# Performance work log

Hardware: AMD Instinct MI355X
Metric: run time of the kernel (lower is better)

Reference implementation:

```python
import jax, jax.numpy as jnp
import numpy as np

EPS = 1e-6


def _csmd(X, M):
    # cross squared Mahalanobis distances: [N, N]
    prod = ((X @ M) * X).sum(axis=1)
    cross = X @ M @ X.T
    return prod[:, None] + prod[None, :] - 2.0 * cross


def setup_inputs() -> dict:
    key = jax.random.key(0)
    kx, kg, ky = jax.random.split(key, 3)
    N, D = 384, 128
    X = jax.random.normal(kx, (N, D), dtype=jnp.float32)
    G = jax.random.normal(kg, (D, D), dtype=jnp.float32)
    y = jax.random.randint(ky, (N,), 0, 10, dtype=jnp.int64)
    return {"X": X, "G": G, "y": y}


def reference(X, G, y):
    N = X.shape[0]
    M = G.T @ G
    csmd = _csmd(X, M)                                  # [N, N]
    # diff[i, j, k] = relu(csmd[i, k] - csmd[i, j])
    diff = jnp.maximum(csmd[:, None, :] - csmd[:, :, None], 0.0)  # [N, N, N]
    csmd2 = _csmd(X, M.T @ M)                           # [N, N]
    denom = jnp.maximum(2.0 * jnp.sqrt(jnp.maximum(csmd2, EPS)), EPS)  # [N, N] over (j, k)
    margins = diff / denom[None, :, :]                  # [N, N, N]
    same = y[None, :] == y[:, None]                     # [N, N], symmetric
    zero_ij = (~same) | jnp.eye(N, dtype=bool)          # zero where y[i]!=y[j] or i==j
    margins = jnp.where(zero_ij[:, :, None], 0.0, margins)
    inner_max = margins.max(axis=1)                     # [N, N] over (i, k)
    inner_max = jnp.where(same, jnp.inf, inner_max)     # exclude same-class k
    return inner_max.min(axis=1)                        # [N]
```

## Files before the change

kernel.cpp:

```cpp
#include <hip/hip_runtime.h>
#include <math.h>

#define NN 384
#define DD 128
#define NTILE (NN / 16)
#define EPSF 1e-6f

__global__ void __launch_bounds__(128) k_A(const float* __restrict__ X,
                                           const float* __restrict__ G,
                                           float* __restrict__ A,
                                           float* __restrict__ prod,
                                           float* __restrict__ p2) {
    __shared__ float Xi[DD];
    __shared__ float Bs[DD];
    __shared__ float rp[2], rq[2];
    const int i = blockIdx.x;
    const int t = threadIdx.x;

    if (t < DD / 4) ((float4*)Xi)[t] = ((const float4*)(X + (size_t)i * DD))[t];
    __syncthreads();

    float b = 0.f;
    const float* gr = G + (size_t)t * DD;
#pragma unroll
    for (int d = 0; d < DD; d += 4) {
        float4 g = *(const float4*)(gr + d);
        b = fmaf(g.x, Xi[d + 0], b);
        b = fmaf(g.y, Xi[d + 1], b);
        b = fmaf(g.z, Xi[d + 2], b);
        b = fmaf(g.w, Xi[d + 3], b);
    }
    Bs[t] = b;
    __syncthreads();

    float a = 0.f;
#pragma unroll 8
    for (int c = 0; c < DD; ++c)
        a = fmaf(Bs[c], G[(size_t)c * DD + t], a);
    A[(size_t)i * DD + t] = a;

    float pp = b * b, qq = a * a;
#pragma unroll
    for (int off = 32; off > 0; off >>= 1) {
        pp += __shfl_down(pp, off);
        qq += __shfl_down(qq, off);
    }
    if ((t & 63) == 0) { rp[t >> 6] = pp; rq[t >> 6] = qq; }
    __syncthreads();
    if (t == 0) { prod[i] = rp[0] + rp[1]; p2[i] = rq[0] + rq[1]; }
}

__global__ void __launch_bounds__(256) k_csmd(const float* __restrict__ X,
                                              const float* __restrict__ A,
                                              const float* __restrict__ prod,
                                              const float* __restrict__ p2,
                                              float* __restrict__ csmd,
                                              float* __restrict__ invd) {
    const int ti = blockIdx.y, tk = blockIdx.x;
    if (ti > tk) return;
    __shared__ float Ai[16][20], Xk[16][20], Ak[16][20];
    __shared__ float Tc[16][17], Tv[16][17];
    const int tx = threadIdx.x, ty = threadIdx.y;
    const int k0 = tk * 16, i0 = ti * 16;
    float dA = 0.f, dAA = 0.f;
    for (int d0 = 0; d0 < DD; d0 += 16) {
        Ai[ty][tx] = A[(size_t)(i0 + ty) * DD + d0 + tx];
        Xk[ty][tx] = X[(size_t)(k0 + ty) * DD + d0 + tx];
        Ak[ty][tx] = A[(size_t)(k0 + ty) * DD + d0 + tx];
        __syncthreads();
#pragma unroll
        for (int t4 = 0; t4 < 16; t4 += 4) {
            float4 aa = *(const float4*)&Ai[ty][t4];
            float4 xx = *(const float4*)&Xk[tx][t4];
            float4 ak = *(const float4*)&Ak[tx][t4];
            dA  = fmaf(aa.x, xx.x, dA);  dA  = fmaf(aa.y, xx.y, dA);
            dA  = fmaf(aa.z, xx.z, dA);  dA  = fmaf(aa.w, xx.w, dA);
            dAA = fmaf(aa.x, ak.x, dAA); dAA = fmaf(aa.y, ak.y, dAA);
            dAA = fmaf(aa.z, ak.z, dAA); dAA = fmaf(aa.w, ak.w, dAA);
        }
        __syncthreads();
    }
    const int i = i0 + ty, k = k0 + tx;
    const float c1 = prod[i] + prod[k] - 2.f * dA;
    const float c2 = p2[i] + p2[k] - 2.f * dAA;
    const float inv = 1.f / fmaxf(2.f * sqrtf(fmaxf(c2, EPSF)), EPSF);
    csmd[(size_t)i * NN + k] = c1;
    invd[(size_t)i * NN + k] = inv;
    if (ti != tk) {
        Tc[tx][ty] = c1;
        Tv[tx][ty] = inv;
        __syncthreads();
        csmd[(size_t)(k0 + ty) * NN + i0 + tx] = Tc[ty][tx];
        invd[(size_t)(k0 + ty) * NN + i0 + tx] = Tv[ty][tx];
    }
}

__global__ void __launch_bounds__(NN) k_cube(const float* __restrict__ csmd,
                                             const float* __restrict__ invd,
                                             const int* __restrict__ y,
                                             float* __restrict__ out) {
    __shared__ float cvals[NN];
    __shared__ int   jidx[NN];
    __shared__ float red[NN];
    __shared__ int   cnt;
    const int i = blockIdx.x;
    const int t = threadIdx.x;
    const int yi = y[i];
    if (t == 0) cnt = 0;
    __syncthreads();
    const float cit = csmd[(size_t)i * NN + t];
    const int yt = y[t];
    if (yt == yi && t != i) {
        int p = atomicAdd(&cnt, 1);
        cvals[p] = cit;
        jidx[p]  = t;
    }
    __syncthreads();
    const int c = cnt;
    float m = 0.f;
    const float* invcol = invd + t;
    for (int jj = 0; jj < c; ++jj) {
        float dlt = fmaxf(cit - cvals[jj], 0.f);
        m = fmaxf(m, dlt * invcol[(size_t)jidx[jj] * NN]);
    }
    if (yt == yi) m = __builtin_inff();
    red[t] = m;
    __syncthreads();
    if (t < 128) red[t] = fminf(red[t], fminf(red[t + 128], red[t + 256]));
    __syncthreads();
    if (t < 64) {
        float v = fminf(red[t], red[t + 64]);
#pragma unroll
        for (int off = 32; off > 0; off >>= 1)
            v = fminf(v, __shfl_down(v, off));
        if (t == 0) out[i] = v;
    }
}

extern "C" void kernel_launch(void* const* d_in, const int* in_sizes, int n_in,
                              void* d_out, int out_size, void* d_ws, size_t ws_size,
                              hipStream_t stream) {
    const float* X = (const float*)d_in[0];
    const float* G = (const float*)d_in[1];
    const int*   y = (const int*)d_in[2];

    float* ws   = (float*)d_ws;
    float* A    = ws;
    float* prod = A + NN * DD;
    float* p2   = prod + NN;
    float* csmd = p2 + NN;
    float* invd = csmd + NN * NN;
    float* out  = (float*)d_out;

    k_A   <<<dim3(NN), dim3(DD), 0, stream>>>(X, G, A, prod, p2);
    k_csmd<<<dim3(NTILE, NTILE), dim3(16, 16), 0, stream>>>(X, A, prod, p2, csmd, invd);
    k_cube<<<dim3(NN), dim3(NN), 0, stream>>>(csmd, invd, y, out);
}
```

Before: 30.07 us.

## Fuse distance and margin stages into a per-class, per-k-chunk kernel

Replaces the full N×N csmd/invd materialization and the cube kernel with one kernel launched over (k-chunk, class). Each block gathers the rows of one class and recomputes the needed same-class distances and inverse denominators in shared memory, using B = G·x so that x M xᵀ = B·Bᵀ. Per-row minima are combined with a float-as-int atomicMin into an output that k_A first sets to infinity. This drops one launch and the global round trip of two N×N buffers, at the price of redundant GEMM work per block. It also hardcodes 10 classes and a cap of 64 rows per class, beyond which rows are silently truncated.

After: 38.86 us. +29.2%, slower.

```diff
diff --git a/kernel.cpp b/kernel.cpp
--- a/kernel.cpp
+++ b/kernel.cpp
@@ -3,14 +3,20 @@
 
 #define NN 384
 #define DD 128
-#define NTILE (NN / 16)
+#define KCH 16
+#define NCHUNK (NN / KCH)
+#define NCLS 10
+#define CMAX 64
+#define STR 132
 #define EPSF 1e-6f
 
 __global__ void __launch_bounds__(128) k_A(const float* __restrict__ X,
                                            const float* __restrict__ G,
+                                           float* __restrict__ B,
                                            float* __restrict__ A,
                                            float* __restrict__ prod,
-                                           float* __restrict__ p2) {
+                                           float* __restrict__ p2,
+                                           float* __restrict__ out) {
     __shared__ float Xi[DD];
     __shared__ float Bs[DD];
     __shared__ float rp[2], rq[2];
@@ -31,6 +37,7 @@
         b = fmaf(g.w, Xi[d + 3], b);
     }
     Bs[t] = b;
+    B[(size_t)i * DD + t] = b;
     __syncthreads();
 
     float a = 0.f;
@@ -47,93 +54,177 @@
     }
     if ((t & 63) == 0) { rp[t >> 6] = pp; rq[t >> 6] = qq; }
     __syncthreads();
-    if (t == 0) { prod[i] = rp[0] + rp[1]; p2[i] = rq[0] + rq[1]; }
+    if (t == 0) {
+        prod[i] = rp[0] + rp[1];
+        p2[i]   = rq[0] + rq[1];
+        out[i]  = __builtin_inff();
+    }
 }
 
-__global__ void __launch_bounds__(256) k_csmd(const float* __restrict__ X,
-                                              const float* __restrict__ A,
-                                              const float* __restrict__ prod,
-                                              const float* __restrict__ p2,
-                                              float* __restrict__ csmd,
-                                              float* __restrict__ invd) {
-    const int ti = blockIdx.y, tk = blockIdx.x;
-    if (ti > tk) return;
-    __shared__ float Ai[16][20], Xk[16][20], Ak[16][20];
-    __shared__ float Tc[16][17], Tv[16][17];
-    const int tx = threadIdx.x, ty = threadIdx.y;
-    const int k0 = tk * 16, i0 = ti * 16;
-    float dA = 0.f, dAA = 0.f;
-    for (int d0 = 0; d0 < DD; d0 += 16) {
-        Ai[ty][tx] = A[(size_t)(i0 + ty) * DD + d0 + tx];
-        Xk[ty][tx] = X[(size_t)(k0 + ty) * DD + d0 + tx];
-        Ak[ty][tx] = A[(size_t)(k0 + ty) * DD + d0 + tx];
-        __syncthreads();
-#pragma unroll
-        for (int t4 = 0; t4 < 16; t4 += 4) {
-            float4 aa = *(const float4*)&Ai[ty][t4];
-            float4 xx = *(const float4*)&Xk[tx][t4];
-            float4 ak = *(const float4*)&Ak[tx][t4];
-            dA  = fmaf(aa.x, xx.x, dA);  dA  = fmaf(aa.y, xx.y, dA);
-            dA  = fmaf(aa.z, xx.z, dA);  dA  = fmaf(aa.w, xx.w, dA);
-            dAA = fmaf(aa.x, ak.x, dAA); dAA = fmaf(aa.y, ak.y, dAA);
-            dAA = fmaf(aa.z, ak.z, dAA); dAA = fmaf(aa.w, ak.w, dAA);
-        }
-        __syncthreads();
-    }
-    const int i = i0 + ty, k = k0 + tx;
-    const float c1 = prod[i] + prod[k] - 2.f * dA;
-    const float c2 = p2[i] + p2[k] - 2.f * dAA;
-    const float inv = 1.f / fmaxf(2.f * sqrtf(fmaxf(c2, EPSF)), EPSF);
-    csmd[(size_t)i * NN + k] = c1;
-    invd[(size_t)i * NN + k] = inv;
-    if (ti != tk) {
-        Tc[tx][ty] = c1;
-        Tv[tx][ty] = inv;
-        __syncthreads();
-        csmd[(size_t)(k0 + ty) * NN + i0 + tx] = Tc[ty][tx];
-        invd[(size_t)(k0 + ty) * NN + i0 + tx] = Tv[ty][tx];
-    }
-}
-
-__global__ void __launch_bounds__(NN) k_cube(const float* __restrict__ csmd,
-                                             const float* __restrict__ invd,
-                                             const int* __restrict__ y,
-                                             float* __restrict__ out) {
-    __shared__ float cvals[NN];
-    __shared__ int   jidx[NN];
-    __shared__ float red[NN];
+__global__ void __launch_bounds__(256) k_margin(const float* __restrict__ B,
+                                                const float* __restrict__ A,
+                                                const float* __restrict__ prod,
+                                                const float* __restrict__ p2,
+                                                const int* __restrict__ y,
+                                                float* __restrict__ out) {
+    __shared__ float SC[CMAX][STR];
+    __shared__ float SK[KCH][STR];
+    __shared__ float ccc[CMAX][CMAX];
+    __shared__ float cck[CMAX][KCH];
+    __shared__ float ick[CMAX][KCH];
+    __shared__ float pc[CMAX], qc[CMAX];
+    __shared__ float pk[KCH], qk[KCH];
+    __shared__ int   yk[KCH];
+    __shared__ int   list[CMAX];
     __shared__ int   cnt;
-    const int i = blockIdx.x;
-    const int t = threadIdx.x;
-    const int yi = y[i];
+
+    const int t  = threadIdx.x;
+    const int tx = t & 15, ty = t >> 4;
+    const int C  = blockIdx.y;
+    const int k0 = blockIdx.x * KCH;
+
     if (t == 0) cnt = 0;
     __syncthreads();
-    const float cit = csmd[(size_t)i * NN + t];
-    const int yt = y[t];
-    if (yt == yi && t != i) {
-        int p = atomicAdd(&cnt, 1);
-        cvals[p] = cit;
-        jidx[p]  = t;
-    }
-    __syncthreads();
-    const int c = cnt;
-    float m = 0.f;
-    const float* invcol = invd + t;
-    for (int jj = 0; jj < c; ++jj) {
-        float dlt = fmaxf(cit - cvals[jj], 0.f);
-        m = fmaxf(m, dlt * invcol[(size_t)jidx[jj] * NN]);
-    }
-    if (yt == yi) m = __builtin_inff();
-    red[t] = m;
-    __syncthreads();
-    if (t < 128) red[t] = fminf(red[t], fminf(red[t + 128], red[t + 256]));
-    __syncthreads();
-    if (t < 64) {
-        float v = fminf(red[t], red[t + 64]);
-#pragma unroll
-        for (int off = 32; off > 0; off >>= 1)
-            v = fminf(v, __shfl_down(v, off));
-        if (t == 0) out[i] = v;
+    for (int r = t; r < NN; r += 256) {
+        if (y[r] == C) {
+            int p = atomicAdd(&cnt, 1);
+            if (p < CMAX) {
+                list[p] = r;
+                pc[p] = prod[r];
+                qc[p] = p2[r];
+            }
+        }
+    }
+    if (t < KCH) {
+        pk[t] = prod[k0 + t];
+        qk[t] = p2[k0 + t];
+        yk[t] = y[k0 + t];
+    }
+    __syncthreads();
+    const int nc = min(cnt, CMAX);
+
+    for (int idx = t; idx < nc * 32; idx += 256) {
+        int r = idx >> 5, q = idx & 31;
+        *(float4*)&SC[r][q * 4] = ((const float4*)(B + (size_t)list[r] * DD))[q];
+    }
+    for (int idx = t; idx < KCH * 32; idx += 256) {
+        int r = idx >> 5, q = idx & 31;
+        *(float4*)&SK[r][q * 4] = ((const float4*)(B + (size_t)(k0 + r) * DD))[q];
+    }
+    __syncthreads();
+
+    {
+        const int i0 = ty * 4;
+        if (i0 < nc) {
+            float acc[4][4] = {};
+#pragma unroll 2
+            for (int d = 0; d < DD; d += 4) {
+                float4 bi[4], bj[4];
+#pragma unroll
+                for (int a = 0; a < 4; ++a) bi[a] = *(const float4*)&SC[i0 + a][d];
+#pragma unroll
+                for (int rj = 0; rj < 4; ++rj) bj[rj] = *(const float4*)&SC[tx + 16 * rj][d];
+#pragma unroll
+                for (int a = 0; a < 4; ++a)
+#pragma unroll
+                    for (int rj = 0; rj < 4; ++rj) {
+                        acc[a][rj] = fmaf(bi[a].x, bj[rj].x, acc[a][rj]);
+                        acc[a][rj] = fmaf(bi[a].y, bj[rj].y, acc[a][rj]);
+                        acc[a][rj] = fmaf(bi[a].z, bj[rj].z, acc[a][rj]);
+                        acc[a][rj] = fmaf(bi[a].w, bj[rj].w, acc[a][rj]);
+                    }
+            }
+#pragma unroll
+            for (int a = 0; a < 4; ++a) {
+                const int i = i0 + a;
+                if (i < nc)
+#pragma unroll
+                    for (int rj = 0; rj < 4; ++rj) {
+                        const int j = tx + 16 * rj;
+                        ccc[i][j] = pc[i] + pc[j] - 2.f * acc[a][rj];
+                    }
+            }
+        }
+    }
+    {
+        float acc[4] = {};
+#pragma unroll 2
+        for (int d = 0; d < DD; d += 4) {
+            float4 bk = *(const float4*)&SK[tx][d];
+#pragma unroll
+            for (int r = 0; r < 4; ++r) {
+                float4 bi = *(const float4*)&SC[ty + 16 * r][d];
+                acc[r] = fmaf(bi.x, bk.x, acc[r]);
+                acc[r] = fmaf(bi.y, bk.y, acc[r]);
+                acc[r] = fmaf(bi.z, bk.z, acc[r]);
+                acc[r] = fmaf(bi.w, bk.w, acc[r]);
+            }
+        }
+#pragma unroll
+        for (int r = 0; r < 4; ++r) {
+            const int i = ty + 16 * r;
+            if (i < nc) cck[i][tx] = pc[i] + pk[tx] - 2.f * acc[r];
+        }
+    }
+    __syncthreads();
+
+    for (int idx = t; idx < nc * 32; idx += 256) {
+        int r = idx >> 5, q = idx & 31;
+        *(float4*)&SC[r][q * 4] = ((const float4*)(A + (size_t)list[r] * DD))[q];
+    }
+    for (int idx = t; idx < KCH * 32; idx += 256) {
+        int r = idx >> 5, q = idx & 31;
+        *(float4*)&SK[r][q * 4] = ((const float4*)(A + (size_t)(k0 + r) * DD))[q];
+    }
+    if (t < nc) ccc[t][t] = __builtin_inff();
+    __syncthreads();
+
+    {
+        float acc[4] = {};
+#pragma unroll 2
+        for (int d = 0; d < DD; d += 4) {
+            float4 ak = *(const float4*)&SK[tx][d];
+#pragma unroll
+            for (int r = 0; r < 4; ++r) {
+                float4 ai = *(const float4*)&SC[ty + 16 * r][d];
+                acc[r] = fmaf(ai.x, ak.x, acc[r]);
+                acc[r] = fmaf(ai.y, ak.y, acc[r]);
+                acc[r] = fmaf(ai.z, ak.z, acc[r]);
+                acc[r] = fmaf(ai.w, ak.w, acc[r]);
+            }
+        }
+#pragma unroll
+        for (int r = 0; r < 4; ++r) {
+            const int j = ty + 16 * r;
+            if (j < nc) {
+                float c2 = qc[j] + qk[tx] - 2.f * acc[r];
+                ick[j][tx] = 1.f / fmaxf(2.f * sqrtf(fmaxf(c2, EPSF)), EPSF);
+            }
+        }
+    }
+    __syncthreads();
+
+    {
+        const bool kex = (yk[tx] == C);
+#pragma unroll
+        for (int r = 0; r < 4; ++r) {
+            const int i = ty + 16 * r;
+            float m = 0.f;
+            if (i < nc) {
+                const float cik = cck[i][tx];
+#pragma unroll 4
+                for (int j = 0; j < nc; ++j) {
+                    float dlt = fmaxf(cik - ccc[i][j], 0.f);
+                    m = fmaxf(m, dlt * ick[j][tx]);
+                }
+            }
+            if (kex) m = __builtin_inff();
+#pragma unroll
+            for (int off = 1; off < 16; off <<= 1)
+                m = fminf(m, __shfl_xor(m, off));
+            if (tx == 0 && i < nc)
+                atomicMin((int*)&out[list[i]], __float_as_int(m));
+        }
     }
 }
 
@@ -145,14 +236,12 @@
     const int*   y = (const int*)d_in[2];
 
     float* ws   = (float*)d_ws;
-    float* A    = ws;
+    float* B    = ws;
+    float* A    = B + NN * DD;
     float* prod = A + NN * DD;
     float* p2   = prod + NN;
-    float* csmd = p2 + NN;
-    float* invd = csmd + NN * NN;
     float* out  = (float*)d_out;
 
-    k_A   <<<dim3(NN), dim3(DD), 0, stream>>>(X, G, A, prod, p2);
-    k_csmd<<<dim3(NTILE, NTILE), dim3(16, 16), 0, stream>>>(X, A, prod, p2, csmd, invd);
-    k_cube<<<dim3(NN), dim3(NN), 0, stream>>>(csmd, invd, y, out);
+    k_A     <<<dim3(NN), dim3(DD), 0, stream>>>(X, G, B, A, prod, p2, out);
+    k_margin<<<dim3(NCHUNK, NCLS), dim3(256), 0, stream>>>(B, A, prod, p2, y, out);
 }
```

## Fuse distance and cube kernels with a grid barrier and B-based csmd

Applied to the files above, without the earlier changes.

Merges the pairwise distance kernel and the triplet max-min kernel into one persistent launch of 144 blocks. The blocks first compute the inverse-denominator matrix with 32x32 tiles and 2x2 register blocking, then sync across the grid through an atomic counter spin barrier. The csmd matrix is no longer stored; each row is recomputed on the fly from B = G·X (csmd = prod_i + prod_j - 2·B_i·B_j), which removes one kernel launch and a full NxN write and read. The risks are that the spin barrier assumes all 144 blocks are resident at once, and that each row is processed by a single block, which lowers parallelism in the cube phase.

Measured after the change: 54.46 us. +81.1%, slower.

```diff
diff --git a/kernel.cpp b/kernel.cpp
--- a/kernel.cpp
+++ b/kernel.cpp
@@ -3,19 +3,28 @@
 
 #define NN 384
 #define DD 128
-#define NTILE (NN / 16)
 #define EPSF 1e-6f
+#define NB2 144
+#define NT2 384
+#define TS 32
+#define NTG (NN / TS)
+#define STR 136
 
 __global__ void __launch_bounds__(128) k_A(const float* __restrict__ X,
                                            const float* __restrict__ G,
+                                           float* __restrict__ B,
                                            float* __restrict__ A,
                                            float* __restrict__ prod,
-                                           float* __restrict__ p2) {
+                                           float* __restrict__ p2,
+                                           int* __restrict__ bar) {
     __shared__ float Xi[DD];
     __shared__ float Bs[DD];
     __shared__ float rp[2], rq[2];
     const int i = blockIdx.x;
     const int t = threadIdx.x;
+
+    if (i == 0 && t == 0)
+        __hip_atomic_store(bar, 0, __ATOMIC_RELAXED, __HIP_MEMORY_SCOPE_AGENT);
 
     if (t < DD / 4) ((float4*)Xi)[t] = ((const float4*)(X + (size_t)i * DD))[t];
     __syncthreads();
@@ -31,6 +40,7 @@
         b = fmaf(g.w, Xi[d + 3], b);
     }
     Bs[t] = b;
+    B[(size_t)i * DD + t] = b;
     __syncthreads();
 
     float a = 0.f;
@@ -50,90 +60,132 @@
     if (t == 0) { prod[i] = rp[0] + rp[1]; p2[i] = rq[0] + rq[1]; }
 }
 
-__global__ void __launch_bounds__(256) k_csmd(const float* __restrict__ X,
-                                              const float* __restrict__ A,
-                                              const float* __restrict__ prod,
-                                              const float* __restrict__ p2,
-                                              float* __restrict__ csmd,
-                                              float* __restrict__ invd) {
-    const int ti = blockIdx.y, tk = blockIdx.x;
-    if (ti > tk) return;
-    __shared__ float Ai[16][20], Xk[16][20], Ak[16][20];
-    __shared__ float Tc[16][17], Tv[16][17];
-    const int tx = threadIdx.x, ty = threadIdx.y;
-    const int k0 = tk * 16, i0 = ti * 16;
-    float dA = 0.f, dAA = 0.f;
-    for (int d0 = 0; d0 < DD; d0 += 16) {
-        Ai[ty][tx] = A[(size_t)(i0 + ty) * DD + d0 + tx];
-        Xk[ty][tx] = X[(size_t)(k0 + ty) * DD + d0 + tx];
-        Ak[ty][tx] = A[(size_t)(k0 + ty) * DD + d0 + tx];
-        __syncthreads();
-#pragma unroll
-        for (int t4 = 0; t4 < 16; t4 += 4) {
-            float4 aa = *(const float4*)&Ai[ty][t4];
-            float4 xx = *(const float4*)&Xk[tx][t4];
-            float4 ak = *(const float4*)&Ak[tx][t4];
-            dA  = fmaf(aa.x, xx.x, dA);  dA  = fmaf(aa.y, xx.y, dA);
-            dA  = fmaf(aa.z, xx.z, dA);  dA  = fmaf(aa.w, xx.w, dA);
-            dAA = fmaf(aa.x, ak.x, dAA); dAA = fmaf(aa.y, ak.y, dAA);
-            dAA = fmaf(aa.z, ak.z, dAA); dAA = fmaf(aa.w, ak.w, dAA);
-        }
-        __syncthreads();
-    }
-    const int i = i0 + ty, k = k0 + tx;
-    const float c1 = prod[i] + prod[k] - 2.f * dA;
-    const float c2 = p2[i] + p2[k] - 2.f * dAA;
-    const float inv = 1.f / fmaxf(2.f * sqrtf(fmaxf(c2, EPSF)), EPSF);
-    csmd[(size_t)i * NN + k] = c1;
-    invd[(size_t)i * NN + k] = inv;
-    if (ti != tk) {
-        Tc[tx][ty] = c1;
-        Tv[tx][ty] = inv;
-        __syncthreads();
-        csmd[(size_t)(k0 + ty) * NN + i0 + tx] = Tc[ty][tx];
-        invd[(size_t)(k0 + ty) * NN + i0 + tx] = Tv[ty][tx];
-    }
-}
-
-__global__ void __launch_bounds__(NN) k_cube(const float* __restrict__ csmd,
-                                             const float* __restrict__ invd,
-                                             const int* __restrict__ y,
-                                             float* __restrict__ out) {
+__global__ void __launch_bounds__(NT2) k_fused(const float* __restrict__ B,
+                                               const float* __restrict__ A,
+                                               const float* __restrict__ prod,
+                                               const float* __restrict__ p2,
+                                               const int* __restrict__ y,
+                                               float* __restrict__ invd,
+                                               int* __restrict__ bar,
+                                               float* __restrict__ out) {
+    __shared__ float Ais[TS][STR], Aks[TS][STR];
+    __shared__ float Tvs[TS][TS + 1];
+    __shared__ float Bsr[DD];
     __shared__ float cvals[NN];
     __shared__ int   jidx[NN];
-    __shared__ float red[NN];
+    __shared__ float red[NT2];
     __shared__ int   cnt;
-    const int i = blockIdx.x;
     const int t = threadIdx.x;
-    const int yi = y[i];
-    if (t == 0) cnt = 0;
-    __syncthreads();
-    const float cit = csmd[(size_t)i * NN + t];
-    const int yt = y[t];
-    if (yt == yi && t != i) {
-        int p = atomicAdd(&cnt, 1);
-        cvals[p] = cit;
-        jidx[p]  = t;
-    }
-    __syncthreads();
-    const int c = cnt;
-    float m = 0.f;
-    const float* invcol = invd + t;
-    for (int jj = 0; jj < c; ++jj) {
-        float dlt = fmaxf(cit - cvals[jj], 0.f);
-        m = fmaxf(m, dlt * invcol[(size_t)jidx[jj] * NN]);
-    }
-    if (yt == yi) m = __builtin_inff();
-    red[t] = m;
-    __syncthreads();
-    if (t < 128) red[t] = fminf(red[t], fminf(red[t + 128], red[t + 256]));
-    __syncthreads();
-    if (t < 64) {
-        float v = fminf(red[t], red[t + 64]);
-#pragma unroll
-        for (int off = 32; off > 0; off >>= 1)
-            v = fminf(v, __shfl_down(v, off));
-        if (t == 0) out[i] = v;
+    const int bidx = blockIdx.x;
+
+    const int ti = bidx / NTG, tk = bidx % NTG;
+    if (bidx < NTG * NTG && ti <= tk) {
+        const int i0 = ti * TS, k0 = tk * TS;
+        for (int idx = t; idx < TS * (DD / 4); idx += NT2) {
+            const int r = idx >> 5, q = (idx & 31) << 2;
+            *(float4*)&Ais[r][q] = *(const float4*)(A + (size_t)(i0 + r) * DD + q);
+            *(float4*)&Aks[r][q] = *(const float4*)(A + (size_t)(k0 + r) * DD + q);
+        }
+        __syncthreads();
+        if (t < 256) {
+            const int u = t & 15, v = t >> 4;
+            float a00 = 0.f, a01 = 0.f, a10 = 0.f, a11 = 0.f;
+#pragma unroll 4
+            for (int d = 0; d < DD; d += 4) {
+                const float4 i0v = *(const float4*)&Ais[v][d];
+                const float4 i1v = *(const float4*)&Ais[v + 16][d];
+                const float4 k0v = *(const float4*)&Aks[u][d];
+                const float4 k1v = *(const float4*)&Aks[u + 16][d];
+                a00 = fmaf(i0v.x, k0v.x, a00); a00 = fmaf(i0v.y, k0v.y, a00);
+                a00 = fmaf(i0v.z, k0v.z, a00); a00 = fmaf(i0v.w, k0v.w, a00);
+                a01 = fmaf(i0v.x, k1v.x, a01); a01 = fmaf(i0v.y, k1v.y, a01);
+                a01 = fmaf(i0v.z, k1v.z, a01); a01 = fmaf(i0v.w, k1v.w, a01);
+                a10 = fmaf(i1v.x, k0v.x, a10); a10 = fmaf(i1v.y, k0v.y, a10);
+                a10 = fmaf(i1v.z, k0v.z, a10); a10 = fmaf(i1v.w, k0v.w, a10);
+                a11 = fmaf(i1v.x, k1v.x, a11); a11 = fmaf(i1v.y, k1v.y, a11);
+                a11 = fmaf(i1v.z, k1v.z, a11); a11 = fmaf(i1v.w, k1v.w, a11);
+            }
+#pragma unroll
+            for (int a = 0; a < 2; ++a)
+#pragma unroll
+                for (int bb = 0; bb < 2; ++bb) {
+                    const int i = i0 + v + 16 * a;
+                    const int k = k0 + u + 16 * bb;
+                    const float acc = a == 0 ? (bb == 0 ? a00 : a01) : (bb == 0 ? a10 : a11);
+                    const float c2 = p2[i] + p2[k] - 2.f * acc;
+                    const float iv = 1.f / fmaxf(2.f * sqrtf(fmaxf(c2, EPSF)), EPSF);
+                    __hip_atomic_store(&invd[(size_t)i * NN + k], iv,
+                                       __ATOMIC_RELAXED, __HIP_MEMORY_SCOPE_AGENT);
+                    Tvs[v + 16 * a][u + 16 * bb] = iv;
+                }
+        }
+        __syncthreads();
+        if (ti != tk) {
+            for (int idx = t; idx < TS * TS; idx += NT2) {
+                const int r = idx >> 5, c = idx & 31;
+                __hip_atomic_store(&invd[(size_t)(k0 + r) * NN + i0 + c], Tvs[c][r],
+                                   __ATOMIC_RELAXED, __HIP_MEMORY_SCOPE_AGENT);
+            }
+        }
+    }
+
+    __syncthreads();
+    if (t == 0) {
+        __hip_atomic_fetch_add(bar, 1, __ATOMIC_ACQ_REL, __HIP_MEMORY_SCOPE_AGENT);
+        while (__hip_atomic_load(bar, __ATOMIC_ACQUIRE, __HIP_MEMORY_SCOPE_AGENT) < NB2)
+            __builtin_amdgcn_s_sleep(2);
+    }
+    __syncthreads();
+
+    for (int rep = 0; rep < 3; ++rep) {
+        const int i = bidx + rep * NB2;
+        if (i >= NN) break;
+        const int yi = y[i];
+        if (t == 0) cnt = 0;
+        if (t < DD / 4) ((float4*)Bsr)[t] = ((const float4*)(B + (size_t)i * DD))[t];
+        __syncthreads();
+
+        float dot = 0.f;
+        const float* brow = B + (size_t)t * DD;
+#pragma unroll 4
+        for (int d = 0; d < DD; d += 4) {
+            const float4 bv = *(const float4*)(brow + d);
+            dot = fmaf(bv.x, Bsr[d + 0], dot);
+            dot = fmaf(bv.y, Bsr[d + 1], dot);
+            dot = fmaf(bv.z, Bsr[d + 2], dot);
+            dot = fmaf(bv.w, Bsr[d + 3], dot);
+        }
+        const float cit = prod[i] + prod[t] - 2.f * dot;
+        const int yt = y[t];
+        if (yt == yi && t != i) {
+            const int p = atomicAdd(&cnt, 1);
+            cvals[p] = cit;
+            jidx[p]  = t;
+        }
+        __syncthreads();
+        const int c = cnt;
+        float m = 0.f;
+        const float* invcol = invd + t;
+#pragma unroll 4
+        for (int jj = 0; jj < c; ++jj) {
+            const float dlt = fmaxf(cit - cvals[jj], 0.f);
+            const float iv = __hip_atomic_load(&invcol[(size_t)jidx[jj] * NN],
+                                               __ATOMIC_RELAXED, __HIP_MEMORY_SCOPE_AGENT);
+            m = fmaxf(m, dlt * iv);
+        }
+        if (yt == yi) m = __builtin_inff();
+        red[t] = m;
+        __syncthreads();
+        if (t < 128) red[t] = fminf(red[t], fminf(red[t + 128], red[t + 256]));
+        __syncthreads();
+        if (t < 64) {
+            float v = fminf(red[t], red[t + 64]);
+#pragma unroll
+            for (int off = 32; off > 0; off >>= 1)
+                v = fminf(v, __shfl_down(v, off));
+            if (t == 0) out[i] = v;
+        }
+        __syncthreads();
     }
 }
 
@@ -145,14 +197,14 @@
     const int*   y = (const int*)d_in[2];
 
     float* ws   = (float*)d_ws;
-    float* A    = ws;
+    float* B    = ws;
+    float* A    = B + NN * DD;
     float* prod = A + NN * DD;
     float* p2   = prod + NN;
-    float* csmd = p2 + NN;
-    float* invd = csmd + NN * NN;
+    float* invd = p2 + NN;
+    int*   bar  = (int*)(invd + NN * NN);
     float* out  = (float*)d_out;
 
-    k_A   <<<dim3(NN), dim3(DD), 0, stream>>>(X, G, A, prod, p2);
-    k_csmd<<<dim3(NTILE, NTILE), dim3(16, 16), 0, stream>>>(X, A, prod, p2, csmd, invd);
-    k_cube<<<dim3(NN), dim3(NN), 0, stream>>>(csmd, invd, y, out);
+    k_A    <<<dim3(NN), dim3(DD), 0, stream>>>(X, G, B, A, prod, p2, bar);
+    k_fused<<<dim3(NB2), dim3(NT2), 0, stream>>>(B, A, prod, p2, y, invd, bar, out);
 }
```

## Split cube kernel over two k-halves with atomicMin, preload full csmd tiles

Applied to the files above, without the earlier changes.

The cube kernel now runs two blocks per row i, each covering 192 k values, and combines their partial minima with an integer atomicMin on out, which k_A initialises to +inf. The same-class candidate list is capped at CMAX=64, and the inner loop is unrolled by four to overlap the gathered invd loads. k_csmd loads whole 16x128 tiles of A and X into shared memory once instead of looping over 16-wide chunks with a sync each time. B is also written out but never used, and the CMAX cap would silently drop candidates if a class had more than 64 members.

Result: faster. 24.79 us (-17.6%).

```diff
diff --git a/kernel.cpp b/kernel.cpp
--- a/kernel.cpp
+++ b/kernel.cpp
@@ -5,12 +5,16 @@
 #define DD 128
 #define NTILE (NN / 16)
 #define EPSF 1e-6f
+#define STR2 132
+#define CMAX 64
 
 __global__ void __launch_bounds__(128) k_A(const float* __restrict__ X,
                                            const float* __restrict__ G,
+                                           float* __restrict__ B,
                                            float* __restrict__ A,
                                            float* __restrict__ prod,
-                                           float* __restrict__ p2) {
+                                           float* __restrict__ p2,
+                                           float* __restrict__ out) {
     __shared__ float Xi[DD];
     __shared__ float Bs[DD];
     __shared__ float rp[2], rq[2];
@@ -31,6 +35,7 @@
         b = fmaf(g.w, Xi[d + 3], b);
     }
     Bs[t] = b;
+    B[(size_t)i * DD + t] = b;
     __syncthreads();
 
     float a = 0.f;
@@ -47,7 +52,11 @@
     }
     if ((t & 63) == 0) { rp[t >> 6] = pp; rq[t >> 6] = qq; }
     __syncthreads();
-    if (t == 0) { prod[i] = rp[0] + rp[1]; p2[i] = rq[0] + rq[1]; }
+    if (t == 0) {
+        prod[i] = rp[0] + rp[1];
+        p2[i]   = rq[0] + rq[1];
+        out[i]  = __builtin_inff();
+    }
 }
 
 __global__ void __launch_bounds__(256) k_csmd(const float* __restrict__ X,
@@ -58,31 +67,38 @@
                                               float* __restrict__ invd) {
     const int ti = blockIdx.y, tk = blockIdx.x;
     if (ti > tk) return;
-    __shared__ float Ai[16][20], Xk[16][20], Ak[16][20];
+    __shared__ float Ais[16][STR2], Xks[16][STR2], Aks[16][STR2];
     __shared__ float Tc[16][17], Tv[16][17];
-    const int tx = threadIdx.x, ty = threadIdx.y;
-    const int k0 = tk * 16, i0 = ti * 16;
+    const int t = threadIdx.x;
+    const int tx = t & 15, ty = t >> 4;
+    const int i0 = ti * 16, k0 = tk * 16;
+
+    for (int idx = t; idx < 1536; idx += 256) {
+        const int sel = idx >> 9;
+        const int r   = (idx >> 5) & 15;
+        const int q   = (idx & 31) << 2;
+        const float* src = (sel == 0) ? (A + (size_t)(i0 + r) * DD + q)
+                         : (sel == 1) ? (X + (size_t)(k0 + r) * DD + q)
+                                      : (A + (size_t)(k0 + r) * DD + q);
+        float* dst = (sel == 0) ? &Ais[r][q] : (sel == 1) ? &Xks[r][q] : &Aks[r][q];
+        *(float4*)dst = *(const float4*)src;
+    }
+    __syncthreads();
+
     float dA = 0.f, dAA = 0.f;
-    for (int d0 = 0; d0 < DD; d0 += 16) {
-        Ai[ty][tx] = A[(size_t)(i0 + ty) * DD + d0 + tx];
-        Xk[ty][tx] = X[(size_t)(k0 + ty) * DD + d0 + tx];
-        Ak[ty][tx] = A[(size_t)(k0 + ty) * DD + d0 + tx];
-        __syncthreads();
-#pragma unroll
-        for (int t4 = 0; t4 < 16; t4 += 4) {
-            float4 aa = *(const float4*)&Ai[ty][t4];
-            float4 xx = *(const float4*)&Xk[tx][t4];
-            float4 ak = *(const float4*)&Ak[tx][t4];
-            dA  = fmaf(aa.x, xx.x, dA);  dA  = fmaf(aa.y, xx.y, dA);
-            dA  = fmaf(aa.z, xx.z, dA);  dA  = fmaf(aa.w, xx.w, dA);
-            dAA = fmaf(aa.x, ak.x, dAA); dAA = fmaf(aa.y, ak.y, dAA);
-            dAA = fmaf(aa.z, ak.z, dAA); dAA = fmaf(aa.w, ak.w, dAA);
-        }
-        __syncthreads();
+#pragma unroll 8
+    for (int d = 0; d < DD; d += 4) {
+        const float4 aa = *(const float4*)&Ais[ty][d];
+        const float4 xx = *(const float4*)&Xks[tx][d];
+        const float4 ak = *(const float4*)&Aks[tx][d];
+        dA  = fmaf(aa.x, xx.x, dA);  dA  = fmaf(aa.y, xx.y, dA);
+        dA  = fmaf(aa.z, xx.z, dA);  dA  = fmaf(aa.w, xx.w, dA);
+        dAA = fmaf(aa.x, ak.x, dAA); dAA = fmaf(aa.y, ak.y, dAA);
+        dAA = fmaf(aa.z, ak.z, dAA); dAA = fmaf(aa.w, ak.w, dAA);
     }
     const int i = i0 + ty, k = k0 + tx;
-    const float c1 = prod[i] + prod[k] - 2.f * dA;
-    const float c2 = p2[i] + p2[k] - 2.f * dAA;
+    const float c1  = prod[i] + prod[k] - 2.f * dA;
+    const float c2  = p2[i] + p2[k] - 2.f * dAA;
     const float inv = 1.f / fmaxf(2.f * sqrtf(fmaxf(c2, EPSF)), EPSF);
     csmd[(size_t)i * NN + k] = c1;
     invd[(size_t)i * NN + k] = inv;
@@ -95,45 +111,59 @@
     }
 }
 
-__global__ void __launch_bounds__(NN) k_cube(const float* __restrict__ csmd,
-                                             const float* __restrict__ invd,
-                                             const int* __restrict__ y,
-                                             float* __restrict__ out) {
-    __shared__ float cvals[NN];
-    __shared__ int   jidx[NN];
-    __shared__ float red[NN];
+__global__ void __launch_bounds__(192) k_cube(const float* __restrict__ csmd,
+                                              const float* __restrict__ invd,
+                                              const int* __restrict__ y,
+                                              float* __restrict__ out) {
+    __shared__ float cvals[CMAX];
+    __shared__ int   jidx[CMAX];
+    __shared__ float red[192];
     __shared__ int   cnt;
     const int i = blockIdx.x;
+    const int h = blockIdx.y;
     const int t = threadIdx.x;
+    const int k = h * 192 + t;
     const int yi = y[i];
     if (t == 0) cnt = 0;
     __syncthreads();
-    const float cit = csmd[(size_t)i * NN + t];
-    const int yt = y[t];
-    if (yt == yi && t != i) {
-        int p = atomicAdd(&cnt, 1);
-        cvals[p] = cit;
-        jidx[p]  = t;
+
+    for (int r = t; r < NN; r += 192) {
+        const float cr = csmd[(size_t)i * NN + r];
+        if (y[r] == yi && r != i) {
+            const int p = atomicAdd(&cnt, 1);
+            if (p < CMAX) { cvals[p] = cr; jidx[p] = r; }
+        }
     }
     __syncthreads();
-    const int c = cnt;
+    const int c = min(cnt, CMAX);
+
+    const float cit = csmd[(size_t)i * NN + k];
+    const int   yk  = y[k];
     float m = 0.f;
-    const float* invcol = invd + t;
-    for (int jj = 0; jj < c; ++jj) {
-        float dlt = fmaxf(cit - cvals[jj], 0.f);
-        m = fmaxf(m, dlt * invcol[(size_t)jidx[jj] * NN]);
+    const float* invcol = invd + k;
+    int jj = 0;
+    for (; jj + 4 <= c; jj += 4) {
+        const float v0 = invcol[(size_t)jidx[jj + 0] * NN];
+        const float v1 = invcol[(size_t)jidx[jj + 1] * NN];
+        const float v2 = invcol[(size_t)jidx[jj + 2] * NN];
+        const float v3 = invcol[(size_t)jidx[jj + 3] * NN];
+        m = fmaxf(m, fmaxf(cit - cvals[jj + 0], 0.f) * v0);
+        m = fmaxf(m, fmaxf(cit - cvals[jj + 1], 0.f) * v1);
+        m = fmaxf(m, fmaxf(cit - cvals[jj + 2], 0.f) * v2);
+        m = fmaxf(m, fmaxf(cit - cvals[jj + 3], 0.f) * v3);
     }
-    if (yt == yi) m = __builtin_inff();
+    for (; jj < c; ++jj)
+        m = fmaxf(m, fmaxf(cit - cvals[jj], 0.f) * invcol[(size_t)jidx[jj] * NN]);
+
+    if (yk == yi) m = __builtin_inff();
     red[t] = m;
     __syncthreads();
-    if (t < 128) red[t] = fminf(red[t], fminf(red[t + 128], red[t + 256]));
-    __syncthreads();
     if (t < 64) {
-        float v = fminf(red[t], red[t + 64]);
+        float v = fminf(red[t], fminf(red[t + 64], red[t + 128]));
 #pragma unroll
         for (int off = 32; off > 0; off >>= 1)
             v = fminf(v, __shfl_down(v, off));
-        if (t == 0) out[i] = v;
+        if (t == 0) atomicMin((int*)&out[i], __float_as_int(v));
     }
 }
 
@@ -145,14 +175,15 @@
     const int*   y = (const int*)d_in[2];
 
     float* ws   = (float*)d_ws;
-    float* A    = ws;
+    float* B    = ws;
+    float* A    = B + NN * DD;
     float* prod = A + NN * DD;
     float* p2   = prod + NN;
     float* csmd = p2 + NN;
     float* invd = csmd + NN * NN;
     float* out  = (float*)d_out;
 
-    k_A   <<<dim3(NN), dim3(DD), 0, stream>>>(X, G, A, prod, p2);
-    k_csmd<<<dim3(NTILE, NTILE), dim3(16, 16), 0, stream>>>(X, A, prod, p2, csmd, invd);
-    k_cube<<<dim3(NN), dim3(NN), 0, stream>>>(csmd, invd, y, out);
+    k_A   <<<dim3(NN), dim3(DD), 0, stream>>>(X, G, B, A, prod, p2, out);
+    k_csmd<<<dim3(NTILE, NTILE), dim3(256), 0, stream>>>(X, A, prod, p2, csmd, invd);
+    k_cube<<<dim3(NN, 2), dim3(192), 0, stream>>>(csmd, invd, y, out);
 }
```
